# Kernel optimization log

Hardware: AMD Instinct MI355X
Metric: run time of the kernel (lower is better)

Reference implementation:

```python
import jax, jax.numpy as jnp
import numpy as np
import math

EMBED_DIM = 2048
NUM_HEADS = 16
HEAD_DIM = EMBED_DIM // NUM_HEADS
BATCH = 4
SEQ = 2048


def setup_inputs() -> dict:
    key = jax.random.key(0)
    ks = jax.random.split(key, 5)
    scale_qkv = 1.0 / math.sqrt(EMBED_DIM)
    x = jax.random.normal(ks[0], (BATCH, SEQ, EMBED_DIM), dtype=jnp.float32)
    w_qkv = jax.random.normal(ks[1], (3 * EMBED_DIM, EMBED_DIM), dtype=jnp.float32) * scale_qkv
    b_qkv = jnp.zeros((3 * EMBED_DIM,), dtype=jnp.float32)
    w_o = jax.random.normal(ks[2], (EMBED_DIM, EMBED_DIM), dtype=jnp.float32) * scale_qkv
    b_o = jnp.zeros((EMBED_DIM,), dtype=jnp.float32)
    return {"x": x, "w_qkv": w_qkv, "b_qkv": b_qkv, "w_o": w_o, "b_o": b_o}


def reference(x, w_qkv, b_qkv, w_o, b_o):
    B, S, D = x.shape
    # fused QKV projection: [B,S,3D]
    qkv = jnp.einsum('bsd,ed->bse', x, w_qkv) + b_qkv
    qkv = qkv.reshape(B, S, 3, NUM_HEADS, HEAD_DIM)
    qkv = jnp.transpose(qkv, (2, 0, 3, 1, 4))  # [3,B,H,S,hd]
    q, k, v = qkv[0], qkv[1], qkv[2]
    scores = jnp.einsum('bhqd,bhkd->bhqk', q, k) / math.sqrt(HEAD_DIM)
    probs = jax.nn.softmax(scores, axis=-1)
    out = jnp.einsum('bhqk,bhkd->bhqd', probs, v)
    out = jnp.transpose(out, (0, 2, 1, 3)).reshape(B, S, D)
    return jnp.einsum('bsd,ed->bse', out, w_o) + b_o
```

## Files before the change

### kernel.cpp

```cpp
#include <hip/hip_runtime.h>
#include <cstdint>
#include <cstddef>

typedef __attribute__((ext_vector_type(8))) __bf16 bf16x8;
typedef __attribute__((ext_vector_type(4))) float f32x4;
typedef __attribute__((ext_vector_type(4))) unsigned short u16x4;
typedef unsigned short u16;

#define BATCH 4
#define SEQ 2048
#define DIM 2048
#define NH 16
#define HD 128
#define BH (BATCH*NH)
#define MROWS (BATCH*SEQ)

__device__ static inline u16 f2bf(float f) {
  union { float f; uint32_t u; } v; v.f = f;
  uint32_t r = v.u + 0x7fffu + ((v.u >> 16) & 1u);
  return (u16)(r >> 16);
}

__device__ static inline uint32_t pkbf(float lo, float hi) {
  union { float f; uint32_t u; } a, b;
  a.f = lo; b.f = hi;
  return __builtin_amdgcn_perm(b.u + 0x8000u, a.u + 0x8000u, 0x07060302u);
}

__device__ static inline void gload_lds16(const void* g, void* l) {
  __builtin_amdgcn_global_load_lds(
      (const __attribute__((address_space(1))) unsigned int*)g,
      (__attribute__((address_space(3))) unsigned int*)l, 16, 0, 0);
}

__device__ static inline f32x4 mfma_bf16(bf16x8 a, bf16x8 b, f32x4 c) {
  return __builtin_amdgcn_mfma_f32_16x16x32_bf16(a, b, c, 0, 0, 0);
}

__global__ __launch_bounds__(256) void cvt_f32_bf16_kernel(
    const float4* __restrict__ in, u16x4* __restrict__ out, int n4, int nscale4,
    float scale) {
  int i = blockIdx.x * 256 + threadIdx.x;
  if (i < n4) {
    float4 f = in[i];
    float s = (i < nscale4) ? scale : 1.0f;
    u16x4 o = { f2bf(f.x * s), f2bf(f.y * s), f2bf(f.z * s), f2bf(f.w * s) };
    out[i] = o;
  }
}

__global__ __launch_bounds__(256) void bias_scale_kernel(
    const float* __restrict__ b, float* __restrict__ out, int n, int nscale,
    float scale) {
  int i = blockIdx.x * 256 + threadIdx.x;
  if (i < n) out[i] = b[i] * ((i < nscale) ? scale : 1.0f);
}

template<int EPI>
__global__ __launch_bounds__(256) void gemm_bt_kernel(
    const u16* __restrict__ A, const u16* __restrict__ W,
    const float* __restrict__ bias, float* __restrict__ Cout,
    int M, int N, int K,
    u16* __restrict__ qb, u16* __restrict__ kb, u16* __restrict__ vtb) {
  __shared__ __align__(16) char lds[65536];

  const int tid = threadIdx.x;
  const int wave = tid >> 6, lane = tid & 63;
  const int quad = lane >> 4, ln = lane & 15;
  const int wm = wave >> 1, wn = wave & 1;
  const int mbase = blockIdx.y * 128;
  const int nbase = blockIdx.x * 128;

  f32x4 acc[4][4];
#pragma unroll
  for (int i = 0; i < 4; i++)
#pragma unroll
    for (int j = 0; j < 4; j++) acc[i][j] = (f32x4){0.f, 0.f, 0.f, 0.f};

  const int chunk0 = wave * 256 + lane;
  const u16* gAp[4]; const u16* gWp[4]; int ldsOff[4];
#pragma unroll
  for (int s = 0; s < 4; s++) {
    int chunk = chunk0 + s * 64;
    int row = chunk >> 3, c = chunk & 7;
    int gc = c ^ (row & 7);
    gAp[s] = A + (size_t)(mbase + row) * K + gc * 8;
    gWp[s] = W + (size_t)(nbase + row) * K + gc * 8;
    ldsOff[s] = chunk * 16;
  }

#pragma unroll
  for (int s = 0; s < 4; s++) {
    gload_lds16(gAp[s], lds + ldsOff[s]);
    gload_lds16(gWp[s], lds + 16384 + ldsOff[s]);
  }

  const int NT = K >> 6;
  for (int kt = 0; kt < NT; kt++) {
    {
      int t = (kt + 1) & (NT - 1);
      char* sbuf = lds + ((kt + 1) & 1) * 32768;
#pragma unroll
      for (int s = 0; s < 4; s++) {
        gload_lds16(gAp[s] + t * 64, sbuf + ldsOff[s]);
        gload_lds16(gWp[s] + t * 64, sbuf + 16384 + ldsOff[s]);
      }
    }
    asm volatile("s_waitcnt vmcnt(8)\n\ts_barrier" ::: "memory");

    const char* ldsA = lds + (kt & 1) * 32768;
    const char* ldsB = ldsA + 16384;

#pragma unroll
    for (int ks = 0; ks < 2; ks++) {
      bf16x8 af[4], bfr[4];
#pragma unroll
      for (int i = 0; i < 4; i++) {
        int row = wm * 64 + i * 16 + ln;
        int ch = (ks * 4 + quad) ^ (row & 7);
        af[i] = *(const bf16x8*)(ldsA + row * 128 + ch * 16);
        int rowb = wn * 64 + i * 16 + ln;
        int chb = (ks * 4 + quad) ^ (rowb & 7);
        bfr[i] = *(const bf16x8*)(ldsB + rowb * 128 + chb * 16);
      }
#pragma unroll
      for (int i = 0; i < 4; i++)
#pragma unroll
        for (int j = 0; j < 4; j++)
          acc[i][j] = mfma_bf16(af[i], bfr[j], acc[i][j]);
    }
    asm volatile("s_waitcnt lgkmcnt(0)\n\ts_barrier" ::: "memory");
  }

  if (EPI == 0 || (nbase >> 11) < 2) {
#pragma unroll
    for (int i = 0; i < 4; i++) {
#pragma unroll
      for (int j = 0; j < 4; j++) {
        int col = nbase + wn * 64 + j * 16 + ln;
        float bv = bias[col];
#pragma unroll
        for (int r = 0; r < 4; r++) {
          int row = mbase + wm * 64 + i * 16 + quad * 4 + r;
          float val = acc[i][j][r] + bv;
          if (EPI == 0) {
            Cout[(size_t)row * N + col] = val;
          } else {
            int b = row >> 11, s = row & 2047;
            int m3 = col >> 11, h = (col >> 7) & 15, d = col & 127;
            int bh = b * NH + h;
            u16 bfv = f2bf(val);
            if (m3 == 0) qb[((size_t)bh * SEQ + s) * HD + d] = bfv;
            else         kb[((size_t)bh * SEQ + s) * HD + d] = bfv;
          }
        }
      }
    }
  } else {
    asm volatile("s_waitcnt vmcnt(0)" ::: "memory");
    __syncthreads();
    int h = (nbase >> 7) & 15;
    int b = mbase >> 11, s0 = mbase & 2047;
    int bh = b * NH + h;
#pragma unroll
    for (int i = 0; i < 4; i++) {
      int sl = wm * 64 + i * 16 + quad * 4;
      int cs = sl >> 3;
      int half = (quad & 1);
#pragma unroll
      for (int j = 0; j < 4; j++) {
        int d = wn * 64 + j * 16 + ln;
        float bv = bias[nbase + d];
        uint2 w2;
        w2.x = pkbf(acc[i][j][0] + bv, acc[i][j][1] + bv);
        w2.y = pkbf(acc[i][j][2] + bv, acc[i][j][3] + bv);
        int cc = cs ^ (d & 15);
        *(uint2*)(lds + d * 256 + cc * 16 + half * 8) = w2;
      }
    }
    __syncthreads();
    u16* vdst = vtb + (size_t)bh * HD * SEQ + s0;
#pragma unroll
    for (int it = 0; it < 8; it++) {
      int chunk = it * 256 + tid;
      int d = chunk >> 4, cc = chunk & 15;
      f32x4 val = *(const f32x4*)(lds + d * 256 + ((cc ^ (d & 15)) * 16));
      *(f32x4*)(vdst + (size_t)d * SEQ + cc * 8) = val;
    }
  }
}

__global__ __launch_bounds__(256, 2) void attn_kernel(
    const u16* __restrict__ Q, const u16* __restrict__ Km,
    const u16* __restrict__ Vt, u16* __restrict__ Out) {
  __shared__ __align__(16) char lds[81920];
  char* ldsP = lds + 65536;

  const int tid = threadIdx.x;
  const int wave = tid >> 6, lane = tid & 63;
  const int quad = lane >> 4, ln = lane & 15;
  const int bh = blockIdx.y;
  const int q0 = blockIdx.x * 128;

  const u16* Qb = Q + (size_t)bh * SEQ * HD;
  const u16* Kb = Km + (size_t)bh * SEQ * HD;
  const u16* Vb = Vt + (size_t)bh * HD * SEQ;

  bf16x8 qf[2][4];
#pragma unroll
  for (int nt = 0; nt < 2; nt++)
#pragma unroll
    for (int ks = 0; ks < 4; ks++) {
      int row = q0 + wave * 32 + nt * 16 + ln;
      qf[nt][ks] = *(const bf16x8*)(Qb + (size_t)row * HD + ks * 32 + quad * 8);
    }

  f32x4 oacc[8][2];
#pragma unroll
  for (int mt = 0; mt < 8; mt++)
#pragma unroll
    for (int nt = 0; nt < 2; nt++) oacc[mt][nt] = (f32x4){0.f, 0.f, 0.f, 0.f};
  float l_s[2] = {0.f, 0.f};

  char* Pw = ldsP + wave * 4096;

  const int chunk0 = wave * 256 + lane;
  const u16* gKp[4]; const u16* gVp[4]; int ldsOff[4];
#pragma unroll
  for (int s4 = 0; s4 < 4; s4++) {
    int chunk = chunk0 + s4 * 64;
    int rk = chunk >> 4, ck = chunk & 15;
    int gk = ck ^ (rk & 15);
    gKp[s4] = Kb + (size_t)rk * HD + gk * 8;
    int rv = chunk >> 3, cv = chunk & 7;
    int gv = cv ^ (rv & 7);
    gVp[s4] = Vb + (size_t)rv * SEQ + gv * 8;
    ldsOff[s4] = chunk * 16;
  }

#pragma unroll
  for (int s4 = 0; s4 < 4; s4++) {
    gload_lds16(gKp[s4], lds + ldsOff[s4]);
    gload_lds16(gVp[s4], lds + 16384 + ldsOff[s4]);
  }

  for (int kt = 0; kt < SEQ / 64; kt++) {
    {
      int t = (kt + 1) & (SEQ / 64 - 1);
      char* buf = lds + ((kt + 1) & 1) * 32768;
#pragma unroll
      for (int s4 = 0; s4 < 4; s4++) {
        gload_lds16(gKp[s4] + (size_t)t * 64 * HD, buf + ldsOff[s4]);
        gload_lds16(gVp[s4] + t * 64, buf + 16384 + ldsOff[s4]);
      }
    }
    asm volatile("s_waitcnt vmcnt(8)\n\ts_barrier" ::: "memory");

    const char* ldsK = lds + (kt & 1) * 32768;
    const char* ldsV = ldsK + 16384;

    f32x4 st[4][2];
#pragma unroll
    for (int mt = 0; mt < 4; mt++)
#pragma unroll
      for (int nt = 0; nt < 2; nt++) st[mt][nt] = (f32x4){0.f, 0.f, 0.f, 0.f};
#pragma unroll
    for (int ks = 0; ks < 4; ks++) {
      bf16x8 kf[4];
#pragma unroll
      for (int mt = 0; mt < 4; mt++) {
        int row = mt * 16 + ln;
        int ch = (ks * 4 + quad) ^ (row & 15);
        kf[mt] = *(const bf16x8*)(ldsK + row * 256 + ch * 16);
      }
#pragma unroll
      for (int mt = 0; mt < 4; mt++)
#pragma unroll
        for (int nt = 0; nt < 2; nt++)
          st[mt][nt] = mfma_bf16(kf[mt], qf[nt][ks], st[mt][nt]);
    }

#pragma unroll
    for (int nt = 0; nt < 2; nt++) {
      float lp = 0.f;
      u16* prow = (u16*)(Pw + (nt * 16 + ln) * 128);
#pragma unroll
      for (int mt = 0; mt < 4; mt++) {
        float p0 = exp2f(st[mt][nt][0] - 4.0f);
        float p1 = exp2f(st[mt][nt][1] - 4.0f);
        float p2 = exp2f(st[mt][nt][2] - 4.0f);
        float p3 = exp2f(st[mt][nt][3] - 4.0f);
        lp += (p0 + p1) + (p2 + p3);
        uint2 w2;
        w2.x = pkbf(p0, p1);
        w2.y = pkbf(p2, p3);
        int cc = (mt * 2 + (quad >> 1)) ^ (ln & 7);
        *(uint2*)((char*)prow + cc * 16 + (quad & 1) * 8) = w2;
      }
      l_s[nt] += lp;
    }
    asm volatile("s_waitcnt lgkmcnt(0)" ::: "memory");

#pragma unroll
    for (int ks2 = 0; ks2 < 2; ks2++) {
      bf16x8 pb[2];
#pragma unroll
      for (int nt = 0; nt < 2; nt++) {
        int cc = (ks2 * 4 + quad) ^ (ln & 7);
        pb[nt] = *(const bf16x8*)(Pw + (nt * 16 + ln) * 128 + cc * 16);
      }
      bf16x8 vf[8];
#pragma unroll
      for (int mt = 0; mt < 8; mt++) {
        int row = mt * 16 + ln;
        int ch = (ks2 * 4 + quad) ^ (row & 7);
        vf[mt] = *(const bf16x8*)(ldsV + row * 128 + ch * 16);
      }
#pragma unroll
      for (int mt = 0; mt < 8; mt++)
#pragma unroll
        for (int nt = 0; nt < 2; nt++)
          oacc[mt][nt] = mfma_bf16(vf[mt], pb[nt], oacc[mt][nt]);
    }
    asm volatile("s_waitcnt lgkmcnt(0)\n\ts_barrier" ::: "memory");
  }

  float inv[2];
#pragma unroll
  for (int nt = 0; nt < 2; nt++) {
    float l = l_s[nt];
    l += __shfl_xor(l, 16);
    l += __shfl_xor(l, 32);
    inv[nt] = 1.0f / l;
  }

  int b = bh >> 4, h = bh & 15;
#pragma unroll
  for (int nt = 0; nt < 2; nt++) {
    int srow = q0 + wave * 32 + nt * 16 + ln;
    size_t base = ((size_t)b * SEQ + srow) * DIM + h * HD;
#pragma unroll
    for (int mt = 0; mt < 8; mt++) {
      int d = mt * 16 + quad * 4;
      u16x4 o = { f2bf(oacc[mt][nt][0] * inv[nt]), f2bf(oacc[mt][nt][1] * inv[nt]),
                  f2bf(oacc[mt][nt][2] * inv[nt]), f2bf(oacc[mt][nt][3] * inv[nt]) };
      *(u16x4*)(Out + base + d) = o;
    }
  }
}

extern "C" void kernel_launch(void* const* d_in, const int* in_sizes, int n_in,
                              void* d_out, int out_size, void* d_ws, size_t ws_size,
                              hipStream_t stream) {
  const float* x     = (const float*)d_in[0];
  const float* w_qkv = (const float*)d_in[1];
  const float* b_qkv = (const float*)d_in[2];
  const float* w_o   = (const float*)d_in[3];
  const float* b_o   = (const float*)d_in[4];
  float* out = (float*)d_out;

  char* ws = (char*)d_ws;
  const size_t SZ_XBF  = (size_t)MROWS * DIM * 2;
  const size_t SZ_WQKV = (size_t)3 * DIM * DIM * 2;
  const size_t SZ_WO   = (size_t)DIM * DIM * 2;
  const size_t SZ_HEAD = (size_t)BH * SEQ * HD * 2;
  u16* x_bf    = (u16*)(ws);
  u16* wqkv_bf = (u16*)(ws + SZ_XBF);
  u16* wo_bf   = (u16*)(ws + SZ_XBF + SZ_WQKV);
  u16* qbuf    = (u16*)(ws + SZ_XBF + SZ_WQKV + SZ_WO);
  u16* kbuf    = (u16*)(ws + SZ_XBF + SZ_WQKV + SZ_WO + SZ_HEAD);
  u16* vtbuf   = (u16*)(ws + SZ_XBF + SZ_WQKV + SZ_WO + 2 * SZ_HEAD);
  float* bq_s  = (float*)(ws + SZ_XBF + SZ_WQKV + SZ_WO + 3 * SZ_HEAD);
  u16* attn_out = x_bf;

  (void)in_sizes; (void)n_in; (void)out_size; (void)ws_size;

  const float scale2 = (float)(0.08838834764831845 * 1.4426950408889634);

  {
    int n4 = MROWS * DIM / 4;
    cvt_f32_bf16_kernel<<<(n4 + 255) / 256, 256, 0, stream>>>(
        (const float4*)x, (u16x4*)x_bf, n4, 0, 1.0f);
    n4 = 3 * DIM * DIM / 4;
    cvt_f32_bf16_kernel<<<(n4 + 255) / 256, 256, 0, stream>>>(
        (const float4*)w_qkv, (u16x4*)wqkv_bf, n4, DIM * DIM / 4, scale2);
    n4 = DIM * DIM / 4;
    cvt_f32_bf16_kernel<<<(n4 + 255) / 256, 256, 0, stream>>>(
        (const float4*)w_o, (u16x4*)wo_bf, n4, 0, 1.0f);
    bias_scale_kernel<<<(3 * DIM + 255) / 256, 256, 0, stream>>>(
        b_qkv, bq_s, 3 * DIM, DIM, scale2);
  }

  gemm_bt_kernel<1><<<dim3(3 * DIM / 128, MROWS / 128), 256, 0, stream>>>(
      x_bf, wqkv_bf, bq_s, nullptr, MROWS, 3 * DIM, DIM, qbuf, kbuf, vtbuf);

  attn_kernel<<<dim3(SEQ / 128, BH), 256, 0, stream>>>(
      qbuf, kbuf, vtbuf, attn_out);

  gemm_bt_kernel<0><<<dim3(DIM / 128, MROWS / 128), 256, 0, stream>>>(
      attn_out, wo_bf, b_o, out, MROWS, DIM, DIM, nullptr, nullptr, nullptr);
}
```

Before: 516.8 us.

## Replace 128x128 GEMMs with 256x256-tile 512-thread kernel using staged prefetch pipeline

Both projection GEMMs move from 128x128 tiles with 4 waves to 256x256 tiles with 8 waves and 128KB of double-buffered LDS. The k-loop is split into four quarter-tile MFMA phases, each overlapping global-to-LDS loads of the next tile, with s_setprio raised around the MFMA phases. Workgroup indices are remapped across XCDs, and the V-transpose epilogue is widened to match. The aim is more operand reuse per LDS byte and better hiding of memory latency. The trade-offs are more barriers per iteration, fewer workgroups for the smaller output GEMM, and heavier LDS use that limits occupancy.

```diff
diff --git a/kernel.cpp b/kernel.cpp
--- a/kernel.cpp
+++ b/kernel.cpp
@@ -14,6 +14,8 @@
 #define HD 128
 #define BH (BATCH*NH)
 #define MROWS (BATCH*SEQ)
+#define KDIM 2048
+#define NTK (KDIM/64)
 
 __device__ static inline u16 f2bf(float f) {
   union { float f; uint32_t u; } v; v.f = f;
@@ -57,137 +59,197 @@
 }
 
 template<int EPI>
-__global__ __launch_bounds__(256) void gemm_bt_kernel(
+__global__ __launch_bounds__(512, 2) void gemm256_kernel(
     const u16* __restrict__ A, const u16* __restrict__ W,
     const float* __restrict__ bias, float* __restrict__ Cout,
-    int M, int N, int K,
+    int N, int nbx,
     u16* __restrict__ qb, u16* __restrict__ kb, u16* __restrict__ vtb) {
-  __shared__ __align__(16) char lds[65536];
+  __shared__ __align__(16) char lds[131072];
 
   const int tid = threadIdx.x;
   const int wave = tid >> 6, lane = tid & 63;
   const int quad = lane >> 4, ln = lane & 15;
-  const int wm = wave >> 1, wn = wave & 1;
-  const int mbase = blockIdx.y * 128;
-  const int nbase = blockIdx.x * 128;
-
-  f32x4 acc[4][4];
-#pragma unroll
-  for (int i = 0; i < 4; i++)
-#pragma unroll
-    for (int j = 0; j < 4; j++) acc[i][j] = (f32x4){0.f, 0.f, 0.f, 0.f};
-
-  const int chunk0 = wave * 256 + lane;
-  const u16* gAp[4]; const u16* gWp[4]; int ldsOff[4];
-#pragma unroll
-  for (int s = 0; s < 4; s++) {
-    int chunk = chunk0 + s * 64;
+  const int qwm = wave >> 2, qwn = wave & 3;
+
+  const int nwg = gridDim.x;
+  const int wg = (blockIdx.x & 7) * (nwg >> 3) + (blockIdx.x >> 3);
+  const int bx = wg % nbx, by = wg / nbx;
+  const int mbase = by * 256, nbase = bx * 256;
+
+  f32x4 acc[2][4][2][2];
+#pragma unroll
+  for (int a = 0; a < 2; a++)
+#pragma unroll
+    for (int i = 0; i < 4; i++)
+#pragma unroll
+      for (int c = 0; c < 2; c++)
+#pragma unroll
+        for (int j = 0; j < 2; j++) acc[a][i][c][j] = (f32x4){0.f, 0.f, 0.f, 0.f};
+
+  const u16* aSrc[2]; const u16* wSrc[2]; int ldsOff[2];
+#pragma unroll
+  for (int s = 0; s < 2; s++) {
+    int chunk = tid + s * 512;
     int row = chunk >> 3, c = chunk & 7;
     int gc = c ^ (row & 7);
-    gAp[s] = A + (size_t)(mbase + row) * K + gc * 8;
-    gWp[s] = W + (size_t)(nbase + row) * K + gc * 8;
+    aSrc[s] = A + (size_t)(mbase + row) * KDIM + gc * 8;
+    wSrc[s] = W + (size_t)(nbase + row) * KDIM + gc * 8;
     ldsOff[s] = chunk * 16;
   }
 
-#pragma unroll
-  for (int s = 0; s < 4; s++) {
-    gload_lds16(gAp[s], lds + ldsOff[s]);
-    gload_lds16(gWp[s], lds + 16384 + ldsOff[s]);
-  }
-
-  const int NT = K >> 6;
-  for (int kt = 0; kt < NT; kt++) {
-    {
-      int t = (kt + 1) & (NT - 1);
-      char* sbuf = lds + ((kt + 1) & 1) * 32768;
-#pragma unroll
-      for (int s = 0; s < 4; s++) {
-        gload_lds16(gAp[s] + t * 64, sbuf + ldsOff[s]);
-        gload_lds16(gWp[s] + t * 64, sbuf + 16384 + ldsOff[s]);
-      }
-    }
-    asm volatile("s_waitcnt vmcnt(8)\n\ts_barrier" ::: "memory");
-
-    const char* ldsA = lds + (kt & 1) * 32768;
-    const char* ldsB = ldsA + 16384;
-
-#pragma unroll
-    for (int ks = 0; ks < 2; ks++) {
-      bf16x8 af[4], bfr[4];
-#pragma unroll
-      for (int i = 0; i < 4; i++) {
-        int row = wm * 64 + i * 16 + ln;
-        int ch = (ks * 4 + quad) ^ (row & 7);
-        af[i] = *(const bf16x8*)(ldsA + row * 128 + ch * 16);
-        int rowb = wn * 64 + i * 16 + ln;
-        int chb = (ks * 4 + quad) ^ (rowb & 7);
-        bfr[i] = *(const bf16x8*)(ldsB + rowb * 128 + chb * 16);
-      }
+  auto stA = [&](int h, int t, int b) {
+#pragma unroll
+    for (int s = 0; s < 2; s++)
+      gload_lds16(aSrc[s] + h * (128 * KDIM) + t * 64,
+                  lds + b * 65536 + h * 16384 + ldsOff[s]);
+  };
+  auto stB = [&](int h, int t, int b) {
+#pragma unroll
+    for (int s = 0; s < 2; s++)
+      gload_lds16(wSrc[s] + h * (128 * KDIM) + t * 64,
+                  lds + b * 65536 + 32768 + h * 16384 + ldsOff[s]);
+  };
+
+  stA(0, 0, 0); stB(0, 0, 0); stB(1, 0, 0); stA(1, 0, 0); stA(0, 1, 1);
+  asm volatile("s_waitcnt vmcnt(6)\n\ts_barrier" ::: "memory");
+
+  bf16x8 af[4][2];
+  bf16x8 bfr[2][2][2];
+
+#define MFMA16(MH, NH)                                                        \
+  __builtin_amdgcn_s_setprio(1);                                              \
+  _Pragma("unroll")                                                           \
+  for (int i = 0; i < 4; i++)                                                 \
+    _Pragma("unroll")                                                         \
+    for (int j = 0; j < 2; j++)                                               \
+      _Pragma("unroll")                                                       \
+      for (int ks = 0; ks < 2; ks++)                                          \
+        acc[MH][i][NH][j] =                                                   \
+            mfma_bf16(af[i][ks], bfr[NH][j][ks], acc[MH][i][NH][j]);          \
+  __builtin_amdgcn_s_setprio(0);
+
+#pragma unroll 2
+  for (int kt = 0; kt < NTK; kt++) {
+    const char* bufc = lds + (kt & 1) * 65536;
+    const int tn = (kt + 1) & (NTK - 1);
+    const int bn = (kt + 1) & 1;
+
+#pragma unroll
+    for (int i = 0; i < 4; i++) {
+      int r = qwm * 64 + i * 16 + ln;
+#pragma unroll
+      for (int ks = 0; ks < 2; ks++)
+        af[i][ks] = *(const bf16x8*)(bufc + r * 128 +
+                                     (((ks * 4 + quad) ^ (r & 7)) * 16));
+    }
+#pragma unroll
+    for (int j = 0; j < 2; j++) {
+      int r = qwn * 32 + j * 16 + ln;
+#pragma unroll
+      for (int ks = 0; ks < 2; ks++)
+        bfr[0][j][ks] = *(const bf16x8*)(bufc + 32768 + r * 128 +
+                                         (((ks * 4 + quad) ^ (r & 7)) * 16));
+    }
+    stB(0, tn, bn);
+    asm volatile("s_waitcnt vmcnt(6)\n\ts_barrier" ::: "memory");
+    MFMA16(0, 0)
+    asm volatile("s_barrier" ::: "memory");
+
+#pragma unroll
+    for (int j = 0; j < 2; j++) {
+      int r = qwn * 32 + j * 16 + ln;
+#pragma unroll
+      for (int ks = 0; ks < 2; ks++)
+        bfr[1][j][ks] = *(const bf16x8*)(bufc + 49152 + r * 128 +
+                                         (((ks * 4 + quad) ^ (r & 7)) * 16));
+    }
+    stB(1, tn, bn);
+    asm volatile("s_waitcnt vmcnt(6)\n\ts_barrier" ::: "memory");
+    MFMA16(0, 1)
+    asm volatile("s_barrier" ::: "memory");
+
+#pragma unroll
+    for (int i = 0; i < 4; i++) {
+      int r = qwm * 64 + i * 16 + ln;
+#pragma unroll
+      for (int ks = 0; ks < 2; ks++)
+        af[i][ks] = *(const bf16x8*)(bufc + 16384 + r * 128 +
+                                     (((ks * 4 + quad) ^ (r & 7)) * 16));
+    }
+    stA(1, tn, bn);
+    asm volatile("s_barrier" ::: "memory");
+    MFMA16(1, 0)
+    asm volatile("s_barrier" ::: "memory");
+
+    stA(0, (kt + 2) & (NTK - 1), kt & 1);
+    asm volatile("s_waitcnt vmcnt(6)\n\ts_barrier" ::: "memory");
+    MFMA16(1, 1)
+    asm volatile("s_barrier" ::: "memory");
+  }
+#undef MFMA16
+
+  if (EPI == 0 || (nbase >> 11) < 2) {
+#pragma unroll
+    for (int Mh = 0; Mh < 2; Mh++)
 #pragma unroll
       for (int i = 0; i < 4; i++)
 #pragma unroll
-        for (int j = 0; j < 4; j++)
-          acc[i][j] = mfma_bf16(af[i], bfr[j], acc[i][j]);
-    }
-    asm volatile("s_waitcnt lgkmcnt(0)\n\ts_barrier" ::: "memory");
-  }
-
-  if (EPI == 0 || (nbase >> 11) < 2) {
-#pragma unroll
-    for (int i = 0; i < 4; i++) {
-#pragma unroll
-      for (int j = 0; j < 4; j++) {
-        int col = nbase + wn * 64 + j * 16 + ln;
-        float bv = bias[col];
-#pragma unroll
-        for (int r = 0; r < 4; r++) {
-          int row = mbase + wm * 64 + i * 16 + quad * 4 + r;
-          float val = acc[i][j][r] + bv;
-          if (EPI == 0) {
-            Cout[(size_t)row * N + col] = val;
-          } else {
-            int b = row >> 11, s = row & 2047;
-            int m3 = col >> 11, h = (col >> 7) & 15, d = col & 127;
-            int bh = b * NH + h;
-            u16 bfv = f2bf(val);
-            if (m3 == 0) qb[((size_t)bh * SEQ + s) * HD + d] = bfv;
-            else         kb[((size_t)bh * SEQ + s) * HD + d] = bfv;
+        for (int Nh = 0; Nh < 2; Nh++)
+#pragma unroll
+          for (int j = 0; j < 2; j++) {
+            int col = nbase + Nh * 128 + qwn * 32 + j * 16 + ln;
+            float bv = bias[col];
+#pragma unroll
+            for (int r = 0; r < 4; r++) {
+              int row = mbase + Mh * 128 + qwm * 64 + i * 16 + quad * 4 + r;
+              float val = acc[Mh][i][Nh][j][r] + bv;
+              if (EPI == 0) {
+                Cout[(size_t)row * N + col] = val;
+              } else {
+                int bb = row >> 11, ss = row & 2047;
+                int h = (col >> 7) & 15, d = col & 127;
+                u16 bfv = f2bf(val);
+                if ((col >> 11) == 0)
+                  qb[((size_t)(bb * NH + h) * SEQ + ss) * HD + d] = bfv;
+                else
+                  kb[((size_t)(bb * NH + h) * SEQ + ss) * HD + d] = bfv;
+              }
+            }
           }
-        }
-      }
-    }
   } else {
     asm volatile("s_waitcnt vmcnt(0)" ::: "memory");
     __syncthreads();
-    int h = (nbase >> 7) & 15;
-    int b = mbase >> 11, s0 = mbase & 2047;
-    int bh = b * NH + h;
-#pragma unroll
-    for (int i = 0; i < 4; i++) {
-      int sl = wm * 64 + i * 16 + quad * 4;
-      int cs = sl >> 3;
-      int half = (quad & 1);
-#pragma unroll
-      for (int j = 0; j < 4; j++) {
-        int d = wn * 64 + j * 16 + ln;
-        float bv = bias[nbase + d];
-        uint2 w2;
-        w2.x = pkbf(acc[i][j][0] + bv, acc[i][j][1] + bv);
-        w2.y = pkbf(acc[i][j][2] + bv, acc[i][j][3] + bv);
-        int cc = cs ^ (d & 15);
-        *(uint2*)(lds + d * 256 + cc * 16 + half * 8) = w2;
-      }
-    }
+    const int b = mbase >> 11, s0 = mbase & 2047;
+    const size_t vrow0 = (size_t)b * DIM + (nbase - 2 * DIM);
+#pragma unroll
+    for (int Mh = 0; Mh < 2; Mh++)
+#pragma unroll
+      for (int i = 0; i < 4; i++) {
+        int s_l = Mh * 128 + qwm * 64 + i * 16 + quad * 4;
+        int sc = s_l >> 3, half = (s_l >> 2) & 1;
+#pragma unroll
+        for (int Nh = 0; Nh < 2; Nh++)
+#pragma unroll
+          for (int j = 0; j < 2; j++) {
+            int d_l = Nh * 128 + qwn * 32 + j * 16 + ln;
+            float bv = bias[nbase + d_l];
+            uint2 w2;
+            w2.x = pkbf(acc[Mh][i][Nh][j][0] + bv, acc[Mh][i][Nh][j][1] + bv);
+            w2.y = pkbf(acc[Mh][i][Nh][j][2] + bv, acc[Mh][i][Nh][j][3] + bv);
+            int cc = sc ^ (d_l & 31);
+            *(uint2*)(lds + d_l * 512 + cc * 16 + half * 8) = w2;
+          }
+      }
     __syncthreads();
-    u16* vdst = vtb + (size_t)bh * HD * SEQ + s0;
-#pragma unroll
-    for (int it = 0; it < 8; it++) {
-      int chunk = it * 256 + tid;
-      int d = chunk >> 4, cc = chunk & 15;
-      f32x4 val = *(const f32x4*)(lds + d * 256 + ((cc ^ (d & 15)) * 16));
-      *(f32x4*)(vdst + (size_t)d * SEQ + cc * 8) = val;
-    }
-  }
+#pragma unroll
+    for (int it = 0; it < 16; it++) {
+      int chunk = it * 512 + tid;
+      int d_l = chunk >> 5, sc2 = chunk & 31;
+      f32x4 val = *(const f32x4*)(lds + d_l * 512 + ((sc2 ^ (d_l & 31)) * 16));
+      *(f32x4*)(vtb + (vrow0 + d_l) * SEQ + s0 + sc2 * 8) = val;
+    }
+  }
+  asm volatile("s_waitcnt vmcnt(0)" ::: "memory");
 }
 
 __global__ __launch_bounds__(256, 2) void attn_kernel(
@@ -391,12 +453,12 @@
         b_qkv, bq_s, 3 * DIM, DIM, scale2);
   }
 
-  gemm_bt_kernel<1><<<dim3(3 * DIM / 128, MROWS / 128), 256, 0, stream>>>(
-      x_bf, wqkv_bf, bq_s, nullptr, MROWS, 3 * DIM, DIM, qbuf, kbuf, vtbuf);
+  gemm256_kernel<1><<<dim3((3 * DIM / 256) * (MROWS / 256)), 512, 0, stream>>>(
+      x_bf, wqkv_bf, bq_s, nullptr, 3 * DIM, 3 * DIM / 256, qbuf, kbuf, vtbuf);
 
   attn_kernel<<<dim3(SEQ / 128, BH), 256, 0, stream>>>(
       qbuf, kbuf, vtbuf, attn_out);
 
-  gemm_bt_kernel<0><<<dim3(DIM / 128, MROWS / 128), 256, 0, stream>>>(
-      attn_out, wo_bf, b_o, out, MROWS, DIM, DIM, nullptr, nullptr, nullptr);
-}
+  gemm256_kernel<0><<<dim3((DIM / 256) * (MROWS / 256)), 512, 0, stream>>>(
+      attn_out, wo_bf, b_o, out, DIM, DIM / 256, nullptr, nullptr, nullptr);
+}
```

After: 453.9 us. 12.2% less time.
